# Optimization experiments

Hardware: AMD Instinct MI355X
Metric: run time of the kernel (lower is better)

The kernel has to match this reference:

```python
import jax, jax.numpy as jnp
import numpy as np

NEG_SLOPE = 0.2

def _gat_layer(x, src, dst, W, a_src, a_dst, bias, concat):
    # x: [N, F_in]; W: [F_in, H*C]; a_src/a_dst: [H, C]; bias: [H*C] or [C]
    N = x.shape[0]
    H, C = a_src.shape
    h = (x @ W).reshape(N, H, C)                      # node features per head
    e_src = jnp.einsum('nhc,hc->nh', h, a_src)        # [N, H]
    e_dst = jnp.einsum('nhc,hc->nh', h, a_dst)        # [N, H]
    e = jax.nn.leaky_relu(e_src[src] + e_dst[dst], NEG_SLOPE)  # [E, H]
    # segment softmax over incoming edges of each destination node
    m = jax.ops.segment_max(e, dst, num_segments=N)   # [N, H]
    p = jnp.exp(e - m[dst])
    denom = jax.ops.segment_sum(p, dst, num_segments=N)
    alpha = p / denom[dst]                            # [E, H]
    msg = h[src] * alpha[:, :, None]                  # [E, H, C]
    out = jax.ops.segment_sum(msg, dst, num_segments=N)  # [N, H, C]
    if concat:
        out = out.reshape(N, H * C) + bias
    else:
        out = out.mean(axis=1) + bias
    return out, alpha


def setup_inputs() -> dict:
    key = jax.random.key(0)
    ks = jax.random.split(key, 12)
    N, E = 20000, 320000
    F_in, Ch, Co, H = 256, 64, 64, 8
    x = jax.random.normal(ks[0], (N, F_in), dtype=jnp.float32)
    edge_index = jax.random.randint(ks[1], (2, E), 0, N, dtype=jnp.int64)
    s = 0.05
    return {
        'x': x,
        'edge_index': edge_index,
        'W1': jax.random.normal(ks[2], (F_in, H * Ch), dtype=jnp.float32) * s,
        'att_src1': jax.random.normal(ks[3], (H, Ch), dtype=jnp.float32) * s,
        'att_dst1': jax.random.normal(ks[4], (H, Ch), dtype=jnp.float32) * s,
        'b1': jnp.zeros((H * Ch,), dtype=jnp.float32),
        'W2': jax.random.normal(ks[5], (H * Ch, H * Co), dtype=jnp.float32) * s,
        'att_src2': jax.random.normal(ks[6], (H, Co), dtype=jnp.float32) * s,
        'att_dst2': jax.random.normal(ks[7], (H, Co), dtype=jnp.float32) * s,
        'b2': jnp.zeros((Co,), dtype=jnp.float32),
    }


def reference(x, edge_index, W1, att_src1, att_dst1, b1, W2, att_src2, att_dst2, b2):
    N = x.shape[0]
    # PyG GATConv adds self-loops by default
    loop = jnp.arange(N, dtype=edge_index.dtype)
    src = jnp.concatenate([edge_index[0], loop])
    dst = jnp.concatenate([edge_index[1], loop])
    h1, alpha1 = _gat_layer(x, src, dst, W1, att_src1, att_dst1, b1, concat=True)
    h1 = jax.nn.relu(h1)
    h2, alpha2 = _gat_layer(h1, src, dst, W2, att_src2, att_dst2, b2, concat=False)
    return h2, alpha1, alpha2
```

## Files before the change

### kernel.cpp

```cpp
#include <hip/hip_runtime.h>

#define H 8
#define C 64
#define HC 512
#define NEG 0.2f

typedef __attribute__((ext_vector_type(8))) short bf16x8;
typedef __attribute__((ext_vector_type(4))) float f32x4;
typedef __attribute__((ext_vector_type(4))) short short4v;
typedef __attribute__((ext_vector_type(8))) short short8v;
typedef __attribute__((ext_vector_type(8))) _Float16 half8v;

__device__ __forceinline__ float leaky(float x) { return x > 0.f ? x : NEG * x; }

__device__ __forceinline__ short f2bf(float x) {
    unsigned u = __float_as_uint(x);
    unsigned r = (u + 0x7fffu + ((u >> 16) & 1u)) >> 16;
    return (short)r;
}
__device__ __forceinline__ float bf2f(short s) {
    return __uint_as_float(((unsigned)(unsigned short)s) << 16);
}

#define GLOAD_LDS16(gp, lp) \
  __builtin_amdgcn_global_load_lds((const __attribute__((address_space(1))) unsigned int*)(gp), \
                                   (__attribute__((address_space(3))) unsigned int*)(lp), 16, 0, 0)

__global__ void k_degree(const int* __restrict__ ei, int E, int N, int* __restrict__ deg) {
    int e = blockIdx.x * blockDim.x + threadIdx.x;
    int Et = E + N;
    if (e >= Et) return;
    int d = (e < E) ? ei[E + e] : (e - E);
    atomicAdd(&deg[d], 1);
}

__global__ __launch_bounds__(1024) void k_scan(const int* __restrict__ deg, int N, int* __restrict__ row_start) {
    __shared__ int part[1024];
    int t = threadIdx.x;
    int chunk = (N + 1023) >> 10;
    int lo = t * chunk, hi = min(lo + chunk, N);
    int s = 0;
    for (int i = lo; i < hi; ++i) s += deg[i];
    part[t] = s;
    __syncthreads();
    for (int off = 1; off < 1024; off <<= 1) {
        int v = (t >= off) ? part[t - off] : 0;
        __syncthreads();
        part[t] += v;
        __syncthreads();
    }
    int base = (t == 0) ? 0 : part[t - 1];
    for (int i = lo; i < hi; ++i) { row_start[i] = base; base += deg[i]; }
    if (t == 1023) row_start[N] = part[1023];
}

__global__ void k_fill(const int* __restrict__ ei, int E, int N,
                       const int* __restrict__ row_start, int* __restrict__ cursor,
                       int* __restrict__ csr_src, int* __restrict__ csr_eid) {
    int e = blockIdx.x * blockDim.x + threadIdx.x;
    int Et = E + N;
    if (e >= Et) return;
    int d, s;
    if (e < E) { s = ei[e]; d = ei[E + e]; } else { s = e - E; d = s; }
    int pos = atomicAdd(&cursor[d], 1);
    int idx = row_start[d] + pos;
    csr_src[idx] = s;
    csr_eid[idx] = e;
}

__global__ void k_split4(const float* __restrict__ in, short* __restrict__ hi,
                         short* __restrict__ lo, int n4) {
    int i = blockIdx.x * blockDim.x + threadIdx.x;
    if (i >= n4) return;
    float4 v = reinterpret_cast<const float4*>(in)[i];
    short4v h, l;
    float vv[4] = {v.x, v.y, v.z, v.w};
    #pragma unroll
    for (int j = 0; j < 4; ++j) {
        short hh = f2bf(vv[j]);
        h[j] = hh;
        l[j] = f2bf(vv[j] - bf2f(hh));
    }
    reinterpret_cast<short4v*>(hi)[i] = h;
    reinterpret_cast<short4v*>(lo)[i] = l;
}

__global__ void k_tsplit(const float* __restrict__ W, short* __restrict__ th,
                         short* __restrict__ tl, int K, int Nc) {
    int idx = blockIdx.x * blockDim.x + threadIdx.x;
    if (idx >= K * Nc) return;
    int c = idx / K, k = idx - c * K;
    float v = W[(long)k * Nc + c];
    short hh = f2bf(v);
    th[idx] = hh;
    tl[idx] = f2bf(v - bf2f(hh));
}

__global__ __launch_bounds__(256) void k_gemm_mfma(const short* __restrict__ Ah, const short* __restrict__ Al,
                                                   const short* __restrict__ Bh, const short* __restrict__ Bl,
                                                   _Float16* __restrict__ Cc, int M, int K,
                                                   const float* __restrict__ a_src, const float* __restrict__ a_dst,
                                                   float* __restrict__ e_src, float* __restrict__ e_dst) {
    __shared__ short lAh[4096], lAl[4096], lBh[4096], lBl[4096];
    int tid = threadIdx.x;
    int w = tid >> 6, lane = tid & 63;
    int wr = w >> 1, wc = w & 1;
    int r0 = blockIdx.x * 128, c0 = blockIdx.y * 128;
    f32x4 acc[4][4] = {};
    int frag_off = ((lane >> 4) * 16 + (lane & 15)) * 8;

    for (int k0 = 0; k0 < K; k0 += 32) {
        __syncthreads();
        #pragma unroll
        for (int it = 0; it < 2; ++it) {
            int slot = it * 256 + tid;
            int rb = slot >> 6, kc = (slot >> 4) & 3, r16 = slot & 15;
            long ga = (long)(r0 + rb * 16 + r16) * K + k0 + kc * 8;
            long gb = (long)(c0 + rb * 16 + r16) * K + k0 + kc * 8;
            int ldst = (it * 256 + w * 64) * 8;
            GLOAD_LDS16(Ah + ga, lAh + ldst);
            GLOAD_LDS16(Al + ga, lAl + ldst);
            GLOAD_LDS16(Bh + gb, lBh + ldst);
            GLOAD_LDS16(Bl + gb, lBl + ldst);
        }
        __syncthreads();
        bf16x8 fah[4], fal[4], fbh[4], fbl[4];
        #pragma unroll
        for (int m = 0; m < 4; ++m) {
            int sa = (wr * 4 + m) * 512 + frag_off;
            fah[m] = *reinterpret_cast<bf16x8*>(&lAh[sa]);
            fal[m] = *reinterpret_cast<bf16x8*>(&lAl[sa]);
            int sb = (wc * 4 + m) * 512 + frag_off;
            fbh[m] = *reinterpret_cast<bf16x8*>(&lBh[sb]);
            fbl[m] = *reinterpret_cast<bf16x8*>(&lBl[sb]);
        }
        #pragma unroll
        for (int m = 0; m < 4; ++m)
            #pragma unroll
            for (int n = 0; n < 4; ++n) {
                acc[m][n] = __builtin_amdgcn_mfma_f32_16x16x32_bf16(fah[m], fbh[n], acc[m][n], 0, 0, 0);
                acc[m][n] = __builtin_amdgcn_mfma_f32_16x16x32_bf16(fah[m], fbl[n], acc[m][n], 0, 0, 0);
                acc[m][n] = __builtin_amdgcn_mfma_f32_16x16x32_bf16(fal[m], fbh[n], acc[m][n], 0, 0, 0);
            }
    }
    int head = blockIdx.y * 2 + wc;
    #pragma unroll
    for (int m = 0; m < 4; ++m)
        #pragma unroll
        for (int j = 0; j < 4; ++j) {
            int gr = r0 + wr * 64 + m * 16 + (lane >> 4) * 4 + j;
            if (gr < M) {
                #pragma unroll
                for (int n = 0; n < 4; ++n)
                    Cc[(long)gr * HC + head * 64 + n * 16 + (lane & 15)] = (_Float16)acc[m][n][j];
            }
        }
    float asv[4], adv[4];
    #pragma unroll
    for (int nn = 0; nn < 4; ++nn) {
        asv[nn] = a_src[head * 64 + nn * 16 + (lane & 15)];
        adv[nn] = a_dst[head * 64 + nn * 16 + (lane & 15)];
    }
    #pragma unroll
    for (int m = 0; m < 4; ++m)
        #pragma unroll
        for (int j = 0; j < 4; ++j) {
            int gr = r0 + wr * 64 + m * 16 + (lane >> 4) * 4 + j;
            float es = 0.f, ed = 0.f;
            #pragma unroll
            for (int nn = 0; nn < 4; ++nn) {
                es = fmaf(acc[m][nn][j], asv[nn], es);
                ed = fmaf(acc[m][nn][j], adv[nn], ed);
            }
            #pragma unroll
            for (int o = 1; o < 16; o <<= 1) {
                es += __shfl_xor(es, o);
                ed += __shfl_xor(ed, o);
            }
            if ((lane & 15) == 0 && gr < M) {
                e_src[gr * 8 + head] = es;
                e_dst[gr * 8 + head] = ed;
            }
        }
}

__global__ __launch_bounds__(512) void k_agg(const half8v* __restrict__ hp8,
                                             const float* __restrict__ e_src,
                                             const float* __restrict__ e_dst,
                                             const int* __restrict__ row_start,
                                             const int* __restrict__ csr_src,
                                             const int* __restrict__ csr_eid,
                                             const float* __restrict__ bias,
                                             float* __restrict__ h2out,
                                             short* __restrict__ h1h,
                                             short* __restrict__ h1l,
                                             float* __restrict__ alpha,
                                             int N, int concat) {
    __shared__ float pbuf[8][512];
    int wid = threadIdx.x >> 6, lane = threadIdx.x & 63;
    int n = blockIdx.x * 8 + wid;
    if (n >= N) return;
    int lo3 = lane & 7, hi3 = lane >> 3;
    int row = row_start[n];
    int deg = row_start[n + 1] - row;
    int chunks = (deg + 7) >> 3;
    bool small = (deg <= 64);
    float* pw = &pbuf[wid][0];
    float ed = e_dst[n * 8 + lo3];
    float psum = 0.f;
    for (int c = 0; c < chunks; ++c) {
        int idx = row + min(c * 8 + lo3, deg - 1);
        int sraw = csr_src[idx];
        int sv = __shfl(sraw, hi3);
        float es = e_src[sv * 8 + lo3];
        float p = __expf(leaky(es + ed));
        if (c * 8 + hi3 >= deg) p = 0.f;
        psum += p;
        if (small) pw[c * 64 + lane] = p;
    }
    psum += __shfl_xor(psum, 8);
    psum += __shfl_xor(psum, 16);
    psum += __shfl_xor(psum, 32);
    float inv = 1.0f / psum;
    float acc[8] = {};
    for (int c = 0; c < chunks; ++c) {
        int idx = row + min(c * 8 + lo3, deg - 1);
        int sraw = csr_src[idx];
        int eidr = csr_eid[idx];
        float p;
        if (small) {
            p = pw[c * 64 + lane];
        } else {
            int sv = __shfl(sraw, hi3);
            float es = e_src[sv * 8 + lo3];
            p = __expf(leaky(es + ed));
            if (c * 8 + hi3 >= deg) p = 0.f;
        }
        int eid = __shfl(eidr, hi3);
        if (c * 8 + hi3 < deg)
            alpha[(long)eid * 8 + lo3] = p * inv;
        #pragma unroll
        for (int eg = 0; eg < 8; ++eg) {
            float pe = __shfl(p, eg * 8 + hi3);
            int   se = __shfl(sraw, eg);
            half8v hv = hp8[(long)se * 64 + lane];
            #pragma unroll
            for (int k = 0; k < 8; ++k)
                acc[k] = fmaf((float)hv[k], pe, acc[k]);
        }
    }
    float invg = __shfl(inv, hi3);
    if (concat) {
        const float4* b4 = reinterpret_cast<const float4*>(bias);
        float4 ba = b4[lane * 2], bb = b4[lane * 2 + 1];
        float bv[8] = {ba.x, ba.y, ba.z, ba.w, bb.x, bb.y, bb.z, bb.w};
        short8v hh, ll;
        #pragma unroll
        for (int k = 0; k < 8; ++k) {
            float v = fmaf(acc[k], invg, bv[k]);
            v = v > 0.f ? v : 0.f;
            short hb = f2bf(v);
            hh[k] = hb;
            ll[k] = f2bf(v - bf2f(hb));
        }
        reinterpret_cast<short8v*>(h1h)[(long)n * 64 + lane] = hh;
        reinterpret_cast<short8v*>(h1l)[(long)n * 64 + lane] = ll;
    } else {
        float sc = invg * 0.125f;
        #pragma unroll
        for (int k = 0; k < 8; ++k) acc[k] *= sc;
        #pragma unroll
        for (int o = 8; o <= 32; o <<= 1)
            #pragma unroll
            for (int k = 0; k < 8; ++k)
                acc[k] += __shfl_xor(acc[k], o);
        if (hi3 == 0) {
            float4 r0, r1;
            r0.x = acc[0] + bias[lo3 * 8 + 0];
            r0.y = acc[1] + bias[lo3 * 8 + 1];
            r0.z = acc[2] + bias[lo3 * 8 + 2];
            r0.w = acc[3] + bias[lo3 * 8 + 3];
            r1.x = acc[4] + bias[lo3 * 8 + 4];
            r1.y = acc[5] + bias[lo3 * 8 + 5];
            r1.z = acc[6] + bias[lo3 * 8 + 6];
            r1.w = acc[7] + bias[lo3 * 8 + 7];
            float4* o4 = reinterpret_cast<float4*>(h2out + (long)n * 64 + lo3 * 8);
            o4[0] = r0;
            o4[1] = r1;
        }
    }
}

extern "C" void kernel_launch(void* const* d_in, const int* in_sizes, int n_in,
                              void* d_out, int out_size, void* d_ws, size_t ws_size,
                              hipStream_t stream) {
    const float* x   = (const float*)d_in[0];
    const int*   ei  = (const int*)d_in[1];
    const float* W1  = (const float*)d_in[2];
    const float* as1 = (const float*)d_in[3];
    const float* ad1 = (const float*)d_in[4];
    const float* b1  = (const float*)d_in[5];
    const float* W2  = (const float*)d_in[6];
    const float* as2 = (const float*)d_in[7];
    const float* ad2 = (const float*)d_in[8];
    const float* b2  = (const float*)d_in[9];

    int N  = in_sizes[0] / 256;
    int E  = in_sizes[1] / 2;
    int Et = E + N;
    int K1 = 256;
    int Mb   = (N + 127) / 128;
    int Mpad = Mb * 128;

    float* out    = (float*)d_out;
    float* h2_out = out;
    float* alpha1 = out + (size_t)N * 64;
    float* alpha2 = alpha1 + (size_t)Et * H;

    _Float16* hpre = (_Float16*)d_ws;
    short* Ahb    = (short*)(hpre + (size_t)Mpad * HC);
    short* Alb    = Ahb + (size_t)Mpad * HC;
    short* W1th   = Alb + (size_t)Mpad * HC;
    short* W1tl   = W1th + (size_t)HC * K1;
    short* W2th   = W1tl + (size_t)HC * K1;
    short* W2tl   = W2th + (size_t)HC * HC;
    float* eS     = (float*)(W2tl + (size_t)HC * HC);
    float* eD     = eS + (size_t)N * H;
    int*   deg    = (int*)(eD + (size_t)N * H);
    int*   cursor = deg + N;
    int*   row_st = cursor + N;
    int*   csr_src= row_st + N + 1;
    int*   csr_eid= csr_src + Et;

    hipMemsetAsync(deg, 0, (size_t)2 * N * sizeof(int), stream);
    int tb = 256;
    k_degree<<<(Et + tb - 1) / tb, tb, 0, stream>>>(ei, E, N, deg);
    k_scan<<<1, 1024, 0, stream>>>(deg, N, row_st);
    k_fill<<<(Et + tb - 1) / tb, tb, 0, stream>>>(ei, E, N, row_st, cursor, csr_src, csr_eid);

    int n4 = N * K1 / 4;
    k_split4<<<(n4 + tb - 1) / tb, tb, 0, stream>>>(x, Ahb, Alb, n4);
    k_tsplit<<<(K1 * HC + tb - 1) / tb, tb, 0, stream>>>(W1, W1th, W1tl, K1, HC);
    k_tsplit<<<(HC * HC + tb - 1) / tb, tb, 0, stream>>>(W2, W2th, W2tl, HC, HC);

    dim3 gg(Mb, HC / 128);
    int gagg = (N + 7) / 8;
    k_gemm_mfma<<<gg, 256, 0, stream>>>(Ahb, Alb, W1th, W1tl, hpre, N, K1, as1, ad1, eS, eD);
    k_agg<<<gagg, 512, 0, stream>>>((const half8v*)hpre, eS, eD, row_st, csr_src, csr_eid,
                                    b1, nullptr, Ahb, Alb, alpha1, N, 1);
    k_gemm_mfma<<<gg, 256, 0, stream>>>(Ahb, Alb, W2th, W2tl, hpre, N, HC, as2, ad2, eS, eD);
    k_agg<<<gagg, 512, 0, stream>>>((const half8v*)hpre, eS, eD, row_st, csr_src, csr_eid,
                                    b2, h2_out, nullptr, nullptr, alpha2, N, 0);
}
```

Measured before the change: 309.1 us.

## Switch GEMM to fp16 with single-precision activations, swizzle blocks, cache CSR indices

The GEMM now uses fp16 MFMA with one fp16 copy of the activations and a hi/lo split of the weights. This needs two MFMAs per tile instead of three bf16 ones and loads one A buffer instead of two. The launch grid becomes 1D with a panel swizzle so that consecutive blocks share row panels, intended to improve L2 reuse. The aggregation kernel prefetches the next chunk's CSR indices and keeps them in LDS for small-degree nodes, so the second pass does not reload them from global memory. Activations are rounded to fp16 only, which lowers accuracy and risks overflow for large values compared with the bf16 hi/lo split.

```diff
diff --git a/kernel.cpp b/kernel.cpp
--- a/kernel.cpp
+++ b/kernel.cpp
@@ -5,22 +5,11 @@
 #define HC 512
 #define NEG 0.2f
 
-typedef __attribute__((ext_vector_type(8))) short bf16x8;
+typedef __attribute__((ext_vector_type(8))) _Float16 half8v;
+typedef __attribute__((ext_vector_type(4))) _Float16 half4v;
 typedef __attribute__((ext_vector_type(4))) float f32x4;
-typedef __attribute__((ext_vector_type(4))) short short4v;
-typedef __attribute__((ext_vector_type(8))) short short8v;
-typedef __attribute__((ext_vector_type(8))) _Float16 half8v;
 
 __device__ __forceinline__ float leaky(float x) { return x > 0.f ? x : NEG * x; }
-
-__device__ __forceinline__ short f2bf(float x) {
-    unsigned u = __float_as_uint(x);
-    unsigned r = (u + 0x7fffu + ((u >> 16) & 1u)) >> 16;
-    return (short)r;
-}
-__device__ __forceinline__ float bf2f(short s) {
-    return __uint_as_float(((unsigned)(unsigned short)s) << 16);
-}
 
 #define GLOAD_LDS16(gp, lp) \
   __builtin_amdgcn_global_load_lds((const __attribute__((address_space(1))) unsigned int*)(gp), \
@@ -68,44 +57,42 @@
     csr_eid[idx] = e;
 }
 
-__global__ void k_split4(const float* __restrict__ in, short* __restrict__ hi,
-                         short* __restrict__ lo, int n4) {
+__global__ void k_tofp16(const float* __restrict__ in, _Float16* __restrict__ out, int n4) {
     int i = blockIdx.x * blockDim.x + threadIdx.x;
     if (i >= n4) return;
     float4 v = reinterpret_cast<const float4*>(in)[i];
-    short4v h, l;
-    float vv[4] = {v.x, v.y, v.z, v.w};
-    #pragma unroll
-    for (int j = 0; j < 4; ++j) {
-        short hh = f2bf(vv[j]);
-        h[j] = hh;
-        l[j] = f2bf(vv[j] - bf2f(hh));
-    }
-    reinterpret_cast<short4v*>(hi)[i] = h;
-    reinterpret_cast<short4v*>(lo)[i] = l;
-}
-
-__global__ void k_tsplit(const float* __restrict__ W, short* __restrict__ th,
-                         short* __restrict__ tl, int K, int Nc) {
+    half4v h;
+    h[0] = (_Float16)v.x; h[1] = (_Float16)v.y;
+    h[2] = (_Float16)v.z; h[3] = (_Float16)v.w;
+    reinterpret_cast<half4v*>(out)[i] = h;
+}
+
+__global__ void k_tsplit(const float* __restrict__ W, _Float16* __restrict__ th,
+                         _Float16* __restrict__ tl, int K, int Nc) {
     int idx = blockIdx.x * blockDim.x + threadIdx.x;
     if (idx >= K * Nc) return;
     int c = idx / K, k = idx - c * K;
     float v = W[(long)k * Nc + c];
-    short hh = f2bf(v);
+    _Float16 hh = (_Float16)v;
     th[idx] = hh;
-    tl[idx] = f2bf(v - bf2f(hh));
-}
-
-__global__ __launch_bounds__(256) void k_gemm_mfma(const short* __restrict__ Ah, const short* __restrict__ Al,
-                                                   const short* __restrict__ Bh, const short* __restrict__ Bl,
-                                                   _Float16* __restrict__ Cc, int M, int K,
+    tl[idx] = (_Float16)(v - (float)hh);
+}
+
+__global__ __launch_bounds__(256) void k_gemm_mfma(const _Float16* __restrict__ A,
+                                                   const _Float16* __restrict__ Bh,
+                                                   const _Float16* __restrict__ Bl,
+                                                   _Float16* __restrict__ Cc, int M, int K, int Pb,
                                                    const float* __restrict__ a_src, const float* __restrict__ a_dst,
                                                    float* __restrict__ e_src, float* __restrict__ e_dst) {
-    __shared__ short lAh[4096], lAl[4096], lBh[4096], lBl[4096];
+    __shared__ _Float16 lA[4096], lBh[4096], lBl[4096];
+    int bid = blockIdx.x;
+    int panel = ((bid >> 5) << 3) + (bid & 7);
+    int colb  = (bid >> 3) & 3;
+    if (panel >= Pb) return;
     int tid = threadIdx.x;
     int w = tid >> 6, lane = tid & 63;
     int wr = w >> 1, wc = w & 1;
-    int r0 = blockIdx.x * 128, c0 = blockIdx.y * 128;
+    int r0 = panel * 128, c0 = colb * 128;
     f32x4 acc[4][4] = {};
     int frag_off = ((lane >> 4) * 16 + (lane & 15)) * 8;
 
@@ -118,32 +105,29 @@
             long ga = (long)(r0 + rb * 16 + r16) * K + k0 + kc * 8;
             long gb = (long)(c0 + rb * 16 + r16) * K + k0 + kc * 8;
             int ldst = (it * 256 + w * 64) * 8;
-            GLOAD_LDS16(Ah + ga, lAh + ldst);
-            GLOAD_LDS16(Al + ga, lAl + ldst);
+            GLOAD_LDS16(A + ga, lA + ldst);
             GLOAD_LDS16(Bh + gb, lBh + ldst);
             GLOAD_LDS16(Bl + gb, lBl + ldst);
         }
         __syncthreads();
-        bf16x8 fah[4], fal[4], fbh[4], fbl[4];
+        half8v fa[4], fbh[4], fbl[4];
         #pragma unroll
         for (int m = 0; m < 4; ++m) {
             int sa = (wr * 4 + m) * 512 + frag_off;
-            fah[m] = *reinterpret_cast<bf16x8*>(&lAh[sa]);
-            fal[m] = *reinterpret_cast<bf16x8*>(&lAl[sa]);
+            fa[m] = *reinterpret_cast<half8v*>(&lA[sa]);
             int sb = (wc * 4 + m) * 512 + frag_off;
-            fbh[m] = *reinterpret_cast<bf16x8*>(&lBh[sb]);
-            fbl[m] = *reinterpret_cast<bf16x8*>(&lBl[sb]);
+            fbh[m] = *reinterpret_cast<half8v*>(&lBh[sb]);
+            fbl[m] = *reinterpret_cast<half8v*>(&lBl[sb]);
         }
         #pragma unroll
         for (int m = 0; m < 4; ++m)
             #pragma unroll
             for (int n = 0; n < 4; ++n) {
-                acc[m][n] = __builtin_amdgcn_mfma_f32_16x16x32_bf16(fah[m], fbh[n], acc[m][n], 0, 0, 0);
-                acc[m][n] = __builtin_amdgcn_mfma_f32_16x16x32_bf16(fah[m], fbl[n], acc[m][n], 0, 0, 0);
-                acc[m][n] = __builtin_amdgcn_mfma_f32_16x16x32_bf16(fal[m], fbh[n], acc[m][n], 0, 0, 0);
-            }
-    }
-    int head = blockIdx.y * 2 + wc;
+                acc[m][n] = __builtin_amdgcn_mfma_f32_16x16x32_f16(fa[m], fbh[n], acc[m][n], 0, 0, 0);
+                acc[m][n] = __builtin_amdgcn_mfma_f32_16x16x32_f16(fa[m], fbl[n], acc[m][n], 0, 0, 0);
+            }
+    }
+    int head = colb * 2 + wc;
     #pragma unroll
     for (int m = 0; m < 4; ++m)
         #pragma unroll
@@ -192,11 +176,12 @@
                                              const int* __restrict__ csr_eid,
                                              const float* __restrict__ bias,
                                              float* __restrict__ h2out,
-                                             short* __restrict__ h1h,
-                                             short* __restrict__ h1l,
+                                             _Float16* __restrict__ h1,
                                              float* __restrict__ alpha,
                                              int N, int concat) {
     __shared__ float pbuf[8][512];
+    __shared__ int   sibuf[8][64];
+    __shared__ int   eibuf[8][64];
     int wid = threadIdx.x >> 6, lane = threadIdx.x & 63;
     int n = blockIdx.x * 8 + wid;
     if (n >= N) return;
@@ -208,10 +193,18 @@
     float* pw = &pbuf[wid][0];
     float ed = e_dst[n * 8 + lo3];
     float psum = 0.f;
+    int idx0 = row + min(lo3, deg - 1);
+    int sraw = csr_src[idx0];
+    int eidr = csr_eid[idx0];
     for (int c = 0; c < chunks; ++c) {
-        int idx = row + min(c * 8 + lo3, deg - 1);
-        int sraw = csr_src[idx];
-        int sv = __shfl(sraw, hi3);
+        int sraw_c = sraw, eidr_c = eidr;
+        if (c + 1 < chunks) {
+            int idxn = row + min((c + 1) * 8 + lo3, deg - 1);
+            sraw = csr_src[idxn];
+            eidr = csr_eid[idxn];
+        }
+        if (small) { sibuf[wid][c * 8 + lo3] = sraw_c; eibuf[wid][c * 8 + lo3] = eidr_c; }
+        int sv = __shfl(sraw_c, hi3);
         float es = e_src[sv * 8 + lo3];
         float p = __expf(leaky(es + ed));
         if (c * 8 + hi3 >= deg) p = 0.f;
@@ -224,25 +217,27 @@
     float inv = 1.0f / psum;
     float acc[8] = {};
     for (int c = 0; c < chunks; ++c) {
-        int idx = row + min(c * 8 + lo3, deg - 1);
-        int sraw = csr_src[idx];
-        int eidr = csr_eid[idx];
-        float p;
+        float p; int sraw_c, eidr_c;
         if (small) {
+            sraw_c = sibuf[wid][c * 8 + lo3];
+            eidr_c = eibuf[wid][c * 8 + lo3];
             p = pw[c * 64 + lane];
         } else {
-            int sv = __shfl(sraw, hi3);
+            int idx = row + min(c * 8 + lo3, deg - 1);
+            sraw_c = csr_src[idx];
+            eidr_c = csr_eid[idx];
+            int sv = __shfl(sraw_c, hi3);
             float es = e_src[sv * 8 + lo3];
             p = __expf(leaky(es + ed));
             if (c * 8 + hi3 >= deg) p = 0.f;
         }
-        int eid = __shfl(eidr, hi3);
+        int eid = __shfl(eidr_c, hi3);
         if (c * 8 + hi3 < deg)
             alpha[(long)eid * 8 + lo3] = p * inv;
         #pragma unroll
         for (int eg = 0; eg < 8; ++eg) {
             float pe = __shfl(p, eg * 8 + hi3);
-            int   se = __shfl(sraw, eg);
+            int   se = __shfl(sraw_c, eg);
             half8v hv = hp8[(long)se * 64 + lane];
             #pragma unroll
             for (int k = 0; k < 8; ++k)
@@ -254,17 +249,14 @@
         const float4* b4 = reinterpret_cast<const float4*>(bias);
         float4 ba = b4[lane * 2], bb = b4[lane * 2 + 1];
         float bv[8] = {ba.x, ba.y, ba.z, ba.w, bb.x, bb.y, bb.z, bb.w};
-        short8v hh, ll;
+        half8v hh;
         #pragma unroll
         for (int k = 0; k < 8; ++k) {
             float v = fmaf(acc[k], invg, bv[k]);
             v = v > 0.f ? v : 0.f;
-            short hb = f2bf(v);
-            hh[k] = hb;
-            ll[k] = f2bf(v - bf2f(hb));
-        }
-        reinterpret_cast<short8v*>(h1h)[(long)n * 64 + lane] = hh;
-        reinterpret_cast<short8v*>(h1l)[(long)n * 64 + lane] = ll;
+            hh[k] = (_Float16)v;
+        }
+        reinterpret_cast<half8v*>(h1)[(long)n * 64 + lane] = hh;
     } else {
         float sc = invg * 0.125f;
         #pragma unroll
@@ -318,12 +310,12 @@
     float* alpha2 = alpha1 + (size_t)Et * H;
 
     _Float16* hpre = (_Float16*)d_ws;
-    short* Ahb    = (short*)(hpre + (size_t)Mpad * HC);
-    short* Alb    = Ahb + (size_t)Mpad * HC;
-    short* W1th   = Alb + (size_t)Mpad * HC;
-    short* W1tl   = W1th + (size_t)HC * K1;
-    short* W2th   = W1tl + (size_t)HC * K1;
-    short* W2tl   = W2th + (size_t)HC * HC;
+    _Float16* h1   = hpre + (size_t)Mpad * HC;
+    _Float16* xh   = h1 + (size_t)Mpad * HC;
+    _Float16* W1th = xh + (size_t)Mpad * K1;
+    _Float16* W1tl = W1th + (size_t)HC * K1;
+    _Float16* W2th = W1tl + (size_t)HC * K1;
+    _Float16* W2tl = W2th + (size_t)HC * HC;
     float* eS     = (float*)(W2tl + (size_t)HC * HC);
     float* eD     = eS + (size_t)N * H;
     int*   deg    = (int*)(eD + (size_t)N * H);
@@ -339,16 +331,17 @@
     k_fill<<<(Et + tb - 1) / tb, tb, 0, stream>>>(ei, E, N, row_st, cursor, csr_src, csr_eid);
 
     int n4 = N * K1 / 4;
-    k_split4<<<(n4 + tb - 1) / tb, tb, 0, stream>>>(x, Ahb, Alb, n4);
+    k_tofp16<<<(n4 + tb - 1) / tb, tb, 0, stream>>>(x, xh, n4);
     k_tsplit<<<(K1 * HC + tb - 1) / tb, tb, 0, stream>>>(W1, W1th, W1tl, K1, HC);
     k_tsplit<<<(HC * HC + tb - 1) / tb, tb, 0, stream>>>(W2, W2th, W2tl, HC, HC);
 
-    dim3 gg(Mb, HC / 128);
+    int Pb8 = ((Mb + 7) / 8) * 8;
+    int ggemm = Pb8 * 4;
     int gagg = (N + 7) / 8;
-    k_gemm_mfma<<<gg, 256, 0, stream>>>(Ahb, Alb, W1th, W1tl, hpre, N, K1, as1, ad1, eS, eD);
+    k_gemm_mfma<<<ggemm, 256, 0, stream>>>(xh, W1th, W1tl, hpre, N, K1, Mb, as1, ad1, eS, eD);
     k_agg<<<gagg, 512, 0, stream>>>((const half8v*)hpre, eS, eD, row_st, csr_src, csr_eid,
-                                    b1, nullptr, Ahb, Alb, alpha1, N, 1);
-    k_gemm_mfma<<<gg, 256, 0, stream>>>(Ahb, Alb, W2th, W2tl, hpre, N, HC, as2, ad2, eS, eD);
+                                    b1, nullptr, h1, alpha1, N, 1);
+    k_gemm_mfma<<<ggemm, 256, 0, stream>>>(h1, W2th, W2tl, hpre, N, HC, Mb, as2, ad2, eS, eD);
     k_agg<<<gagg, 512, 0, stream>>>((const half8v*)hpre, eS, eD, row_st, csr_src, csr_eid,
-                                    b2, h2_out, nullptr, nullptr, alpha2, N, 0);
-}
+                                    b2, h2_out, nullptr, alpha2, N, 0);
+}
```

New measurement: 274.7 us. 1.13x faster.
